# Performance work log

Hardware: AMD Instinct MI355X
Metric: run time of the kernel (lower is better)

## Reference

```python
import jax, jax.numpy as jnp
import numpy as np

N_NODES = 100000
N_EDGES = 1700000


def _build_csr(rng, n, e):
    row = rng.integers(0, n, size=e).astype(np.int64)
    col = rng.integers(0, n, size=e).astype(np.int32)
    order = np.argsort(row, kind='stable')
    row = row[order]
    col = col[order]
    rowptr = np.searchsorted(row, np.arange(n + 1)).astype(np.int32)
    return rowptr, col


def setup_inputs() -> dict:
    key = jax.random.key(0)
    k1, k2, k3, k4 = jax.random.split(key, 4)
    rng = np.random.default_rng(0)
    rowptr, colind = _build_csr(rng, N_NODES, N_EDGES)
    F_in, H, C = 256, 128, 16
    return {
        'x': jax.random.normal(k1, (N_NODES, F_in), dtype=jnp.float32),
        'edge_weight': jax.random.uniform(k2, (N_EDGES,), dtype=jnp.float32) + 0.5,
        'W1': jax.random.normal(k3, (F_in, H), dtype=jnp.float32) * (1.0 / np.sqrt(F_in)),
        'b1': jnp.zeros((H,), dtype=jnp.float32),
        'W2': jax.random.normal(k4, (H, C), dtype=jnp.float32) * (1.0 / np.sqrt(H)),
        'b2': jnp.zeros((C,), dtype=jnp.float32),
        'rowptr': jnp.asarray(rowptr),
        'colind': jnp.asarray(colind),
    }


def _rowids_from_rowptr(rowptr, n_edges):
    # CSR rowptr -> per-nnz row index, jit-friendly
    return (jnp.searchsorted(rowptr, jnp.arange(n_edges, dtype=rowptr.dtype), side='right') - 1).astype(jnp.int32)


def reference(x, edge_weight, W1, b1, W2, b2, rowptr, colind):
    n = x.shape[0]
    e = colind.shape[0]
    row = _rowids_from_rowptr(rowptr, e)
    col = colind

    # GCN symmetric normalization: D^-1/2 A D^-1/2 (cached=True -> shared by both layers)
    deg = jax.ops.segment_sum(edge_weight, row, num_segments=n)
    dinv = jnp.where(deg > 0, jax.lax.rsqrt(deg), 0.0)
    w = dinv[row] * edge_weight * dinv[col]

    def gcn_layer(h, W, b):
        h = h @ W                                   # [n, d_out]
        # SpMM: out[r] = sum_e w[e] * h[col[e]]
        msg = w[:, None] * h[col]                   # [e, d_out] gather
        return jax.ops.segment_sum(msg, row, num_segments=n) + b

    h = jax.nn.relu(gcn_layer(x, W1, b1))
    # dropout is identity in eval mode
    out = gcn_layer(h, W2, b2)
    return jax.nn.log_softmax(out, axis=1)
```

## Files before the change

kernel.cpp:

```cpp
#include <hip/hip_runtime.h>
#include <hip/hip_bf16.h>

#define F_IN 256
#define HDIM 128
#define CDIM 16

typedef unsigned short u16;
typedef unsigned int u32;

typedef __attribute__((ext_vector_type(8))) short bf16x8;
typedef __attribute__((ext_vector_type(4))) float f32x4;

__device__ __forceinline__ float bf2f(u32 v) {
    u32 u = v << 16;
    float f;
    __builtin_memcpy(&f, &u, 4);
    return f;
}
__device__ __forceinline__ u16 f2bf(float f) {
    u32 u;
    __builtin_memcpy(&u, &f, 4);
    u32 r = (u + 0x7FFFu + ((u >> 16) & 1u)) >> 16;
    return (u16)r;
}
__device__ __forceinline__ u32 cvtpk(float lo, float hi) {
    u32 r;
    asm("v_cvt_pk_bf16_f32 %0, %1, %2" : "=v"(r) : "v"(lo), "v"(hi));
    return r;
}

__global__ void k_dinv(const float* __restrict__ ew, const int* __restrict__ rowptr,
                       float* __restrict__ dinv, int n) {
    int r = blockIdx.x * blockDim.x + threadIdx.x;
    if (r >= n) return;
    int s = rowptr[r], e = rowptr[r + 1];
    float acc = 0.f;
    for (int i = s; i < e; i++) acc += ew[i];
    dinv[r] = (acc > 0.f) ? rsqrtf(acc) : 0.f;
}

__global__ void k_w(const float* __restrict__ ew, const int* __restrict__ rowptr,
                    const int* __restrict__ col, const float* __restrict__ dinv,
                    float* __restrict__ wn, int n) {
    int r = blockIdx.x * blockDim.x + threadIdx.x;
    if (r >= n) return;
    float dr = dinv[r];
    int s = rowptr[r], e = rowptr[r + 1];
    for (int i = s; i < e; i++) wn[i] = dr * ew[i] * dinv[col[i]];
}

__global__ void k_prepw1(const float* __restrict__ W1, u16* __restrict__ W1T) {
    int idx = blockIdx.x * blockDim.x + threadIdx.x;
    if (idx >= HDIM * F_IN) return;
    int f = idx >> 8;
    int k = idx & 255;
    W1T[idx] = f2bf(W1[(size_t)k * HDIM + f]);
}

__global__ __launch_bounds__(512, 4) void k_gemm1(const float* __restrict__ x,
                                                  const u16* __restrict__ W1T,
                                                  u16* __restrict__ T1, int n) {
    __shared__ u16 Bs[HDIM * F_IN];

    int tid = threadIdx.x;
#pragma unroll
    for (int it = 0; it < 8; it++) {
        int o16 = it * 512 + tid;
        u32 o = (u32)o16 * 16;
        u32 swz = o ^ (((o >> 9) & 7u) << 4);
        uint4 v = ((const uint4*)W1T)[o16];
        *(uint4*)((char*)Bs + swz) = v;
    }
    __syncthreads();

    int wave = tid >> 6;
    int lane = tid & 63;
    int lr = lane & 15;
    int kg = lane >> 4;
    int r0 = blockIdx.x * 256 + wave * 32;
    if (r0 >= n) return;

    f32x4 acc[2][8];
#pragma unroll
    for (int rg = 0; rg < 2; rg++)
#pragma unroll
        for (int ct = 0; ct < 8; ct++) acc[rg][ct] = (f32x4){0.f, 0.f, 0.f, 0.f};

    int rowc[2];
#pragma unroll
    for (int rg = 0; rg < 2; rg++) {
        int row = r0 + rg * 16 + lr;
        rowc[rg] = row < n ? row : (n - 1);
    }

#pragma unroll
    for (int kk = 0; kk < F_IN / 32; kk++) {
        bf16x8 afrag[2];
#pragma unroll
        for (int rg = 0; rg < 2; rg++) {
            const float4* ap = (const float4*)(x + (size_t)rowc[rg] * F_IN + kg * 8 + kk * 32);
            float4 alo = ap[0];
            float4 ahi = ap[1];
            u32 q0 = cvtpk(alo.x, alo.y);
            u32 q1 = cvtpk(alo.z, alo.w);
            u32 q2 = cvtpk(ahi.x, ahi.y);
            u32 q3 = cvtpk(ahi.z, ahi.w);
            u32 qa[4] = {q0, q1, q2, q3};
            __builtin_memcpy(&afrag[rg], qa, 16);
        }
#pragma unroll
        for (int ct = 0; ct < 8; ct++) {
            u32 a = (u32)(ct * 16 + lr) * (F_IN * 2) + (u32)kg * 16 + (u32)kk * 64;
            u32 aswz = a ^ (((a >> 9) & 7u) << 4);
            bf16x8 bfrag = *(const bf16x8*)((const char*)Bs + aswz);
#pragma unroll
            for (int rg = 0; rg < 2; rg++)
                acc[rg][ct] = __builtin_amdgcn_mfma_f32_16x16x32_bf16(afrag[rg], bfrag, acc[rg][ct], 0, 0, 0);
        }
    }

#pragma unroll
    for (int rg = 0; rg < 2; rg++) {
        int rbase = r0 + rg * 16 + kg * 4;
#pragma unroll
        for (int ct = 0; ct < 8; ct++) {
#pragma unroll
            for (int i = 0; i < 4; i += 2) {
                u32 q = cvtpk(acc[rg][ct][i], acc[rg][ct][i + 1]);
                int row0 = rbase + i;
                int row1 = rbase + i + 1;
                if (row0 < n) T1[(size_t)row0 * HDIM + ct * 16 + lr] = (u16)(q & 0xFFFFu);
                if (row1 < n) T1[(size_t)row1 * HDIM + ct * 16 + lr] = (u16)(q >> 16);
            }
        }
    }
}

__global__ __launch_bounds__(256) void k_spmm1(const u16* __restrict__ T1,
                                               const float* __restrict__ wn,
                                               const int* __restrict__ rowptr,
                                               const int* __restrict__ col,
                                               const float* __restrict__ b1,
                                               u16* __restrict__ H, int n) {
    int wave = threadIdx.x >> 6;
    int lane = threadIdx.x & 63;
    int r = blockIdx.x * 4 + wave;
    if (r >= n) return;
    int es = lane >> 4;
    int fl = lane & 15;

    int s = rowptr[r], e = rowptr[r + 1];
    float a[8];
#pragma unroll
    for (int j = 0; j < 8; j++) a[j] = 0.f;

#define ACCUM(w_, p_) do { \
        a[0] += (w_) * bf2f((p_).x & 0xFFFFu); a[1] += (w_) * bf2f((p_).x >> 16); \
        a[2] += (w_) * bf2f((p_).y & 0xFFFFu); a[3] += (w_) * bf2f((p_).y >> 16); \
        a[4] += (w_) * bf2f((p_).z & 0xFFFFu); a[5] += (w_) * bf2f((p_).z >> 16); \
        a[6] += (w_) * bf2f((p_).w & 0xFFFFu); a[7] += (w_) * bf2f((p_).w >> 16); \
    } while (0)

    int i = s + es;
    for (; i + 12 < e; i += 16) {
        float w0 = wn[i];      int c0 = col[i];
        float w1 = wn[i + 4];  int c1 = col[i + 4];
        float w2 = wn[i + 8];  int c2 = col[i + 8];
        float w3 = wn[i + 12]; int c3 = col[i + 12];
        uint4 p0 = *(const uint4*)(T1 + (size_t)c0 * HDIM + fl * 8);
        uint4 p1 = *(const uint4*)(T1 + (size_t)c1 * HDIM + fl * 8);
        uint4 p2 = *(const uint4*)(T1 + (size_t)c2 * HDIM + fl * 8);
        uint4 p3 = *(const uint4*)(T1 + (size_t)c3 * HDIM + fl * 8);
        ACCUM(w0, p0);
        ACCUM(w1, p1);
        ACCUM(w2, p2);
        ACCUM(w3, p3);
    }
    for (; i < e; i += 4) {
        float w0 = wn[i];
        int c0 = col[i];
        uint4 p0 = *(const uint4*)(T1 + (size_t)c0 * HDIM + fl * 8);
        ACCUM(w0, p0);
    }
#undef ACCUM

#pragma unroll
    for (int j = 0; j < 8; j++) {
        a[j] += __shfl_xor(a[j], 16);
        a[j] += __shfl_xor(a[j], 32);
    }

    if (es == 0) {
        const float4* bb = (const float4*)(b1 + fl * 8);
        float4 blo = bb[0], bhi = bb[1];
        float v0 = a[0] + blo.x, v1 = a[1] + blo.y;
        float v2 = a[2] + blo.z, v3 = a[3] + blo.w;
        float v4 = a[4] + bhi.x, v5 = a[5] + bhi.y;
        float v6 = a[6] + bhi.z, v7 = a[7] + bhi.w;
        v0 = v0 > 0.f ? v0 : 0.f; v1 = v1 > 0.f ? v1 : 0.f;
        v2 = v2 > 0.f ? v2 : 0.f; v3 = v3 > 0.f ? v3 : 0.f;
        v4 = v4 > 0.f ? v4 : 0.f; v5 = v5 > 0.f ? v5 : 0.f;
        v6 = v6 > 0.f ? v6 : 0.f; v7 = v7 > 0.f ? v7 : 0.f;
        uint4 o;
        o.x = cvtpk(v0, v1); o.y = cvtpk(v2, v3);
        o.z = cvtpk(v4, v5); o.w = cvtpk(v6, v7);
        *(uint4*)(H + (size_t)r * HDIM + fl * 8) = o;
    }
}

__global__ __launch_bounds__(256) void k_gemm2(const u16* __restrict__ H,
                                               const float* __restrict__ W2,
                                               float* __restrict__ U, int n) {
    int rl = threadIdx.x >> 4;
    int f = threadIdx.x & 15;
    int row = blockIdx.x * 16 + rl;
    if (row >= n) return;
    const u32* hr = (const u32*)(H + (size_t)row * HDIM);
    float acc = 0.f;
    for (int k2 = 0; k2 < HDIM / 2; k2++) {
        u32 pr = hr[k2];
        float h0 = bf2f(pr & 0xFFFFu);
        float h1 = bf2f(pr >> 16);
        acc += h0 * W2[(size_t)(k2 * 2) * CDIM + f];
        acc += h1 * W2[(size_t)(k2 * 2 + 1) * CDIM + f];
    }
    U[(size_t)row * CDIM + f] = acc;
}

__global__ __launch_bounds__(256) void k_out(const float* __restrict__ U,
                                             const float* __restrict__ wn,
                                             const int* __restrict__ rowptr,
                                             const int* __restrict__ col,
                                             const float* __restrict__ b2,
                                             float* __restrict__ out, int n) {
    int wave = threadIdx.x >> 6;
    int lane = threadIdx.x & 63;
    int r = blockIdx.x * 4 + wave;
    if (r >= n) return;
    int es = lane >> 3;
    int fl = lane & 7;
    int s = rowptr[r], e = rowptr[r + 1];
    float a0 = 0.f, a1 = 0.f;

    int i = s + es;
    for (; i + 8 < e; i += 16) {
        float w0 = wn[i];     int c0 = col[i];
        float w1 = wn[i + 8]; int c1 = col[i + 8];
        float2 u0 = *(const float2*)(U + (size_t)c0 * CDIM + fl * 2);
        float2 u1 = *(const float2*)(U + (size_t)c1 * CDIM + fl * 2);
        a0 += w0 * u0.x; a1 += w0 * u0.y;
        a0 += w1 * u1.x; a1 += w1 * u1.y;
    }
    for (; i < e; i += 8) {
        float w0 = wn[i];
        int c0 = col[i];
        float2 u0 = *(const float2*)(U + (size_t)c0 * CDIM + fl * 2);
        a0 += w0 * u0.x; a1 += w0 * u0.y;
    }

    a0 += __shfl_xor(a0, 8);  a1 += __shfl_xor(a1, 8);
    a0 += __shfl_xor(a0, 16); a1 += __shfl_xor(a1, 16);
    a0 += __shfl_xor(a0, 32); a1 += __shfl_xor(a1, 32);

    float2 bp = ((const float2*)b2)[fl];
    float v0 = a0 + bp.x;
    float v1 = a1 + bp.y;

    float m = fmaxf(v0, v1);
    m = fmaxf(m, __shfl_xor(m, 1));
    m = fmaxf(m, __shfl_xor(m, 2));
    m = fmaxf(m, __shfl_xor(m, 4));
    float ss = __expf(v0 - m) + __expf(v1 - m);
    ss += __shfl_xor(ss, 1);
    ss += __shfl_xor(ss, 2);
    ss += __shfl_xor(ss, 4);
    float ls = __logf(ss);
    if (es == 0) {
        float2 res = {v0 - m - ls, v1 - m - ls};
        *(float2*)(out + (size_t)r * CDIM + fl * 2) = res;
    }
}

extern "C" void kernel_launch(void* const* d_in, const int* in_sizes, int n_in,
                              void* d_out, int out_size, void* d_ws, size_t ws_size,
                              hipStream_t stream) {
    const float* x      = (const float*)d_in[0];
    const float* ew     = (const float*)d_in[1];
    const float* W1     = (const float*)d_in[2];
    const float* b1     = (const float*)d_in[3];
    const float* W2     = (const float*)d_in[4];
    const float* b2     = (const float*)d_in[5];
    const int*   rowptr = (const int*)d_in[6];
    const int*   colind = (const int*)d_in[7];

    int n = in_sizes[6] - 1;
    int E = in_sizes[7];

    auto align256 = [](size_t v) { return (v + 255) & ~(size_t)255; };
    char* p = (char*)d_ws;
    float* dinv = (float*)p; p += align256((size_t)n * 4);
    float* wn   = (float*)p; p += align256((size_t)E * 4);
    u16*   T1   = (u16*)p;   p += align256((size_t)n * HDIM * 2);
    u16*   H    = (u16*)p;   p += align256((size_t)n * HDIM * 2);
    float* U    = (float*)p; p += align256((size_t)n * CDIM * 4);
    u16*   W1T  = (u16*)p;   p += align256((size_t)HDIM * F_IN * 2);
    float* out  = (float*)d_out;

    k_dinv<<<(n + 255) / 256, 256, 0, stream>>>(ew, rowptr, dinv, n);
    k_w<<<(n + 255) / 256, 256, 0, stream>>>(ew, rowptr, colind, dinv, wn, n);
    k_prepw1<<<(HDIM * F_IN + 255) / 256, 256, 0, stream>>>(W1, W1T);

    k_gemm1<<<(n + 255) / 256, 512, 0, stream>>>(x, W1T, T1, n);

    k_spmm1<<<(n + 3) / 4, 256, 0, stream>>>(T1, wn, rowptr, colind, b1, H, n);
    k_gemm2<<<(n + 15) / 16, 256, 0, stream>>>(H, W2, U, n);
    k_out<<<(n + 3) / 4, 256, 0, stream>>>(U, wn, rowptr, colind, b2, out, n);
}
```

Measured before the change: 190.5 us.

## Use 16-lane subgroups per row in degree kernels and predicate SpMM remainder loops

The degree and edge-weight normalization kernels now assign a 16-lane subgroup to each row instead of one thread. The subgroup does strided, coalesced reads and a shuffle reduction, which replaces serial per-thread loops with scattered access. Both SpMM kernels fold their remainder loops into a single predicated unrolled loop, clamping indices so all four gathers stay in flight. The wn and col streams are read with nontemporal loads to reduce cache pollution. This adds wasted lanes for short rows and extra gathers of a clamped duplicate row.

```diff
diff --git a/kernel.cpp b/kernel.cpp
--- a/kernel.cpp
+++ b/kernel.cpp
@@ -29,24 +29,36 @@
     return r;
 }
 
-__global__ void k_dinv(const float* __restrict__ ew, const int* __restrict__ rowptr,
-                       float* __restrict__ dinv, int n) {
-    int r = blockIdx.x * blockDim.x + threadIdx.x;
+__global__ __launch_bounds__(256) void k_dinv(const float* __restrict__ ew,
+                                              const int* __restrict__ rowptr,
+                                              float* __restrict__ dinv, int n) {
+    int sg = threadIdx.x >> 4;
+    int sl = threadIdx.x & 15;
+    int r = blockIdx.x * 16 + sg;
     if (r >= n) return;
     int s = rowptr[r], e = rowptr[r + 1];
     float acc = 0.f;
-    for (int i = s; i < e; i++) acc += ew[i];
-    dinv[r] = (acc > 0.f) ? rsqrtf(acc) : 0.f;
-}
-
-__global__ void k_w(const float* __restrict__ ew, const int* __restrict__ rowptr,
-                    const int* __restrict__ col, const float* __restrict__ dinv,
-                    float* __restrict__ wn, int n) {
-    int r = blockIdx.x * blockDim.x + threadIdx.x;
+    for (int i = s + sl; i < e; i += 16) acc += ew[i];
+    acc += __shfl_xor(acc, 1);
+    acc += __shfl_xor(acc, 2);
+    acc += __shfl_xor(acc, 4);
+    acc += __shfl_xor(acc, 8);
+    if (sl == 0) dinv[r] = (acc > 0.f) ? rsqrtf(acc) : 0.f;
+}
+
+__global__ __launch_bounds__(256) void k_w(const float* __restrict__ ew,
+                                           const int* __restrict__ rowptr,
+                                           const int* __restrict__ col,
+                                           const float* __restrict__ dinv,
+                                           float* __restrict__ wn, int n) {
+    int sg = threadIdx.x >> 4;
+    int sl = threadIdx.x & 15;
+    int r = blockIdx.x * 16 + sg;
     if (r >= n) return;
     float dr = dinv[r];
     int s = rowptr[r], e = rowptr[r + 1];
-    for (int i = s; i < e; i++) wn[i] = dr * ew[i] * dinv[col[i]];
+    for (int i = s + sl; i < e; i += 16)
+        wn[i] = dr * ew[i] * dinv[col[i]];
 }
 
 __global__ void k_prepw1(const float* __restrict__ W1, u16* __restrict__ W1T) {
@@ -161,12 +173,21 @@
         a[6] += (w_) * bf2f((p_).w & 0xFFFFu); a[7] += (w_) * bf2f((p_).w >> 16); \
     } while (0)
 
-    int i = s + es;
-    for (; i + 12 < e; i += 16) {
-        float w0 = wn[i];      int c0 = col[i];
-        float w1 = wn[i + 4];  int c1 = col[i + 4];
-        float w2 = wn[i + 8];  int c2 = col[i + 8];
-        float w3 = wn[i + 12]; int c3 = col[i + 12];
+    for (int i0 = s; i0 < e; i0 += 16) {
+        int i = i0 + es;
+        int i1 = i + 4, i2 = i + 8, i3 = i + 12;
+        int j0 = i  < e ? i  : (e - 1);
+        int j1 = i1 < e ? i1 : (e - 1);
+        int j2 = i2 < e ? i2 : (e - 1);
+        int j3 = i3 < e ? i3 : (e - 1);
+        float w0 = i  < e ? __builtin_nontemporal_load(wn + j0) : 0.f;
+        float w1 = i1 < e ? __builtin_nontemporal_load(wn + j1) : 0.f;
+        float w2 = i2 < e ? __builtin_nontemporal_load(wn + j2) : 0.f;
+        float w3 = i3 < e ? __builtin_nontemporal_load(wn + j3) : 0.f;
+        int c0 = __builtin_nontemporal_load(col + j0);
+        int c1 = __builtin_nontemporal_load(col + j1);
+        int c2 = __builtin_nontemporal_load(col + j2);
+        int c3 = __builtin_nontemporal_load(col + j3);
         uint4 p0 = *(const uint4*)(T1 + (size_t)c0 * HDIM + fl * 8);
         uint4 p1 = *(const uint4*)(T1 + (size_t)c1 * HDIM + fl * 8);
         uint4 p2 = *(const uint4*)(T1 + (size_t)c2 * HDIM + fl * 8);
@@ -175,12 +196,6 @@
         ACCUM(w1, p1);
         ACCUM(w2, p2);
         ACCUM(w3, p3);
-    }
-    for (; i < e; i += 4) {
-        float w0 = wn[i];
-        int c0 = col[i];
-        uint4 p0 = *(const uint4*)(T1 + (size_t)c0 * HDIM + fl * 8);
-        ACCUM(w0, p0);
     }
 #undef ACCUM
 
@@ -242,20 +257,19 @@
     int s = rowptr[r], e = rowptr[r + 1];
     float a0 = 0.f, a1 = 0.f;
 
-    int i = s + es;
-    for (; i + 8 < e; i += 16) {
-        float w0 = wn[i];     int c0 = col[i];
-        float w1 = wn[i + 8]; int c1 = col[i + 8];
+    for (int i0 = s; i0 < e; i0 += 16) {
+        int i = i0 + es;
+        int i1 = i + 8;
+        int j0 = i  < e ? i  : (e - 1);
+        int j1 = i1 < e ? i1 : (e - 1);
+        float w0 = i  < e ? __builtin_nontemporal_load(wn + j0) : 0.f;
+        float w1 = i1 < e ? __builtin_nontemporal_load(wn + j1) : 0.f;
+        int c0 = __builtin_nontemporal_load(col + j0);
+        int c1 = __builtin_nontemporal_load(col + j1);
         float2 u0 = *(const float2*)(U + (size_t)c0 * CDIM + fl * 2);
         float2 u1 = *(const float2*)(U + (size_t)c1 * CDIM + fl * 2);
         a0 += w0 * u0.x; a1 += w0 * u0.y;
         a0 += w1 * u1.x; a1 += w1 * u1.y;
-    }
-    for (; i < e; i += 8) {
-        float w0 = wn[i];
-        int c0 = col[i];
-        float2 u0 = *(const float2*)(U + (size_t)c0 * CDIM + fl * 2);
-        a0 += w0 * u0.x; a1 += w0 * u0.y;
     }
 
     a0 += __shfl_xor(a0, 8);  a1 += __shfl_xor(a1, 8);
@@ -306,8 +320,8 @@
     u16*   W1T  = (u16*)p;   p += align256((size_t)HDIM * F_IN * 2);
     float* out  = (float*)d_out;
 
-    k_dinv<<<(n + 255) / 256, 256, 0, stream>>>(ew, rowptr, dinv, n);
-    k_w<<<(n + 255) / 256, 256, 0, stream>>>(ew, rowptr, colind, dinv, wn, n);
+    k_dinv<<<(n + 15) / 16, 256, 0, stream>>>(ew, rowptr, dinv, n);
+    k_w<<<(n + 15) / 16, 256, 0, stream>>>(ew, rowptr, colind, dinv, wn, n);
     k_prepw1<<<(HDIM * F_IN + 255) / 256, 256, 0, stream>>>(W1, W1T);
 
     k_gemm1<<<(n + 255) / 256, 512, 0, stream>>>(x, W1T, T1, n);
```

Result: slower. 200.4 us (+5.2%).
